# Optimization experiments

Hardware: AMD Instinct MI355X
Metric: run time of the kernel (lower is better)

The kernel has to match this reference:

```python
import jax, jax.numpy as jnp
import numpy as np

ALPHA = 0.25
GAMMA = 2.0
LOG_CLAMP = -100.0  # torch binary_cross_entropy clamps log terms at -100


def _conv_same(x, k, stride):
    # x: NHWC, k: HWIO, TF-style SAME padding
    return jax.lax.conv_general_dilated(
        x, k, window_strides=(stride, stride), padding='SAME',
        dimension_numbers=('NHWC', 'HWIO', 'NHWC'))


def _interp_axis(x, axis, out_size):
    # 1-D linear interpolation with align_corners=True semantics
    in_size = x.shape[axis]
    scale = (in_size - 1) / max(out_size - 1, 1)
    pos = jnp.arange(out_size, dtype=x.dtype) * jnp.asarray(scale, dtype=x.dtype)
    i0 = jnp.floor(pos).astype(jnp.int32)
    i1 = jnp.minimum(i0 + 1, in_size - 1)
    w = pos - i0.astype(x.dtype)
    bshape = [1] * x.ndim
    bshape[axis] = out_size
    w = w.reshape(bshape)
    return jnp.take(x, i0, axis=axis) * (1 - w) + jnp.take(x, i1, axis=axis) * w


def _upsample_bilinear_ac(x, factor):
    # NHWC bilinear upsample, align_corners=True (separable)
    x = _interp_axis(x, 1, x.shape[1] * factor)
    x = _interp_axis(x, 2, x.shape[2] * factor)
    return x


def _focal_loss_sum(p, t):
    # binary_cross_entropy (probabilities, not logits) with torch's -100 log clamp
    log_p = jnp.maximum(jnp.log(p), LOG_CLAMP)
    log_1mp = jnp.maximum(jnp.log(1.0 - p), LOG_CLAMP)
    ce = -(t * log_p + (1.0 - t) * log_1mp)
    p_t = p * t + (1.0 - p) * (1.0 - t)
    alpha_t = ALPHA * t + (1.0 - ALPHA) * (1.0 - t)
    return jnp.sum(alpha_t * ce * (1.0 - p_t) ** GAMMA)


def setup_inputs() -> dict:
    key = jax.random.key(0)
    k1, k2 = jax.random.split(key)
    B, H, W = 32, 512, 512
    network_output = jax.random.uniform(k1, (B, H, W, 1), dtype=jnp.float32)
    targets = jax.random.normal(k2, (B, H, W, 2), dtype=jnp.float32)
    # buffers (constants in the original module)
    lap2d = jnp.array([[-1.0, -1.0, -1.0], [-1.0, 8.0, -1.0], [-1.0, -1.0, -1.0]],
                      dtype=jnp.float32)
    laplacian = jnp.stack((lap2d, lap2d), axis=-1).reshape(3, 3, 2, 1)  # HWIO
    fuse_kernel = jnp.array([0.6, 0.3, 0.1], dtype=jnp.float32).reshape(1, 1, 3, 1)
    return {"network_output": network_output, "targets": targets,
            "laplacian": laplacian, "fuse_kernel": fuse_kernel}


def reference(network_output, targets, laplacian, fuse_kernel):
    t = targets[..., 0:2]                                   # [B,H,W,2]
    dt = t.dtype

    b1 = jnp.clip(_conv_same(t, laplacian, 1), 0.0, 1.0)    # [B,H,W,1]
    b1 = (b1 > 0.1).astype(dt)

    b2 = jnp.clip(_conv_same(t, laplacian, 2), 0.0, 1.0)    # [B,H/2,W/2,1]
    b2 = (_upsample_bilinear_ac(b2, 2) > 0.1).astype(dt)

    b4 = jnp.clip(_conv_same(t, laplacian, 4), 0.0, 1.0)    # [B,H/4,W/4,1]
    b4 = (_upsample_bilinear_ac(b4, 4) > 0.1).astype(dt)

    pyr = jnp.concatenate((b1, b2, b4), axis=-1)            # [B,H,W,3]
    fused = _conv_same(pyr, fuse_kernel, 1)                  # [B,H,W,1]
    fused = (fused > 0.1).astype(dt)

    return _focal_loss_sum(network_output, fused)
```

## Files before the change

kernel.cpp:

```cpp
#include <hip/hip_runtime.h>
#include <math.h>


#define B_ 32
#define H_ 512
#define W_ 512

constexpr int TY = 32;
constexpr int TX = 64;
constexpr int RRY = 37;
constexpr int SSTR = 70;
constexpr int NPAIR = RRY * 35;

__global__ __launch_bounds__(256, 8) void edge_focal_kernel(
    const float* __restrict__ net,
    const float* __restrict__ tgt,
    double* __restrict__ partial)
{
    __shared__ float sT[RRY * SSTR];
    __shared__ float sB2[18 * 36];
    __shared__ double sRed[4];

    const int tid = threadIdx.x;
    const int x0 = blockIdx.x * TX;
    const int y0 = blockIdx.y * TY;
    const int b  = blockIdx.z;

    const int lane = tid & 63;
    const int wv   = tid >> 6;
    const int py0  = wv * 8;
    const int gx   = x0 + lane;

    const float* tb = tgt + (size_t)b * (H_ * W_ * 2);
    const bool interior = (x0 >= 64) && (x0 <= 384) && (y0 >= 32) && (y0 <= 448);
    float4 q[6];
    #pragma unroll
    for (int k = 0; k < 6; ++k) {
        const int idx = tid + k * 256;
        const int r   = idx / 35;
        const int c2  = idx - r * 35;
        const int gy  = y0 - 2 + r;
        const int gxx = x0 - 2 + 2 * c2;
        const int gyc = min(max(gy, 0), H_ - 1);
        const int gxc = min(max(gxx, 0), W_ - 2);
        q[k] = *reinterpret_cast<const float4*>(tb + ((size_t)gyc * W_ + gxc) * 2);
    }

    const float* nb = net + (size_t)b * (H_ * W_);
    float p[8];
    #pragma unroll
    for (int i = 0; i < 8; ++i)
        p[i] = nb[(size_t)(y0 + py0 + i) * W_ + gx];

    #pragma unroll
    for (int k = 0; k < 6; ++k) {
        const int idx = tid + k * 256;
        if (idx < NPAIR) {
            const int r  = idx / 35;
            const int c2 = idx - r * 35;
            float v0, v1;
            if (interior) {
                v0 = q[k].x + q[k].y;
                v1 = q[k].z + q[k].w;
            } else {
                const int gy  = y0 - 2 + r;
                const int gxx = x0 - 2 + 2 * c2;
                const bool oky = (unsigned)gy < (unsigned)H_;
                v0 = (oky && (unsigned)gxx       < (unsigned)W_) ? q[k].x + q[k].y : 0.f;
                v1 = (oky && (unsigned)(gxx + 1) < (unsigned)W_) ? q[k].z + q[k].w : 0.f;
            }
            sT[r * SSTR + 2 * c2]     = v0;
            sT[r * SSTR + 2 * c2 + 1] = v1;
        }
    }
    __syncthreads();

    const float s2 = (float)(255.0 / 511.0);

    const int r2lo = (int)((float)y0 * s2);
    const int c2lo = (int)((float)x0 * s2);
    const int r2hi = min((int)((float)(y0 + TY - 1) * s2) + 1, 255);
    const int c2hi = min((int)((float)(x0 + TX - 1) * s2) + 1, 255);
    const int n2r = r2hi - r2lo + 1, n2c = c2hi - c2lo + 1;

    #pragma unroll
    for (int k = 0; k < 3; ++k) {
        const int idx = tid + k * 256;
        if (idx < 18 * 36) {
            const int rr = idx / 36, cc = idx - rr * 36;
            if (rr < n2r && cc < n2c) {
                const int ly = 2 * (r2lo + rr) - (y0 - 2);
                const int lx = 2 * (c2lo + cc) - (x0 - 2);
                const float* q0 = &sT[ly * SSTR + lx];
                const float* q1 = q0 + SSTR;
                const float* q2 = q1 + SSTR;
                float s9 = q0[0] + q0[1] + q0[2] + q1[0] + q1[1] + q1[2] + q2[0] + q2[1] + q2[2];
                float cv = 9.f * q1[1] - s9;
                sB2[idx] = fminf(fmaxf(cv, 0.f), 1.f);
            }
        }
    }
    __syncthreads();

    const int lx = lane + 2;

    const float posx = (float)gx * s2;
    const int   j0   = (int)posx;
    const int   j1   = min(j0 + 1, 255);
    const float wx   = posx - (float)j0;
    const int   bc0  = j0 - c2lo;
    const bool  xclamp = (j1 == j0);

    const float* row = &sT[(py0 + 1) * SSTR + lx - 1];
    float rs_m = row[0] + row[1] + row[2];
    row += SSTR;
    float c_c = row[1];
    float rs_c = row[0] + c_c + row[2];

    float facc = 0.f;
    #pragma unroll
    for (int i = 0; i < 8; ++i) {
        const int py = py0 + i;
        const int gy = y0 + py;
        row = &sT[(py + 3) * SSTR + lx - 1];
        const float n0 = row[0], n1 = row[1], n2 = row[2];
        const float rs_p = n0 + n1 + n2;

        const float cv1 = 9.f * c_c - (rs_m + rs_c + rs_p);
        const bool e1 = cv1 > 0.1f;

        const float posy = (float)gy * s2;
        const int   i0   = (int)posy;
        const int   i1   = min(i0 + 1, 255);
        const float wy   = posy - (float)i0;
        const int   a0   = i0 - r2lo, a1 = i1 - r2lo;
        const float v00 = sB2[a0 * 36 + bc0];
        const float v01r = sB2[a0 * 36 + bc0 + 1];
        const float v10 = sB2[a1 * 36 + bc0];
        const float v11r = sB2[a1 * 36 + bc0 + 1];
        const float v01 = xclamp ? v00 : v01r;
        const float v11 = xclamp ? v10 : v11r;
        const float ta  = v00 * (1.f - wy) + v10 * wy;
        const float tb2 = v01 * (1.f - wy) + v11 * wy;
        const float v2  = ta * (1.f - wx) + tb2 * wx;
        const bool e2 = v2 > 0.1f;

        const bool pos = e1 || e2;
        const float pv = p[i];
        const float qv = pos ? pv : 1.f - pv;
        const float al = pos ? 0.25f : 0.75f;
        const float lg = fmaxf(__logf(qv), -100.f);
        const float om = 1.f - qv;
        facc += al * (-lg) * (om * om);

        rs_m = rs_c; rs_c = rs_p; c_c = n1;
    }

    #pragma unroll
    for (int off = 32; off > 0; off >>= 1)
        facc += __shfl_down(facc, off);
    if (lane == 0) sRed[wv] = (double)facc;
    __syncthreads();
    if (tid == 0) {
        partial[((size_t)blockIdx.z * gridDim.y + blockIdx.y) * gridDim.x + blockIdx.x] =
            sRed[0] + sRed[1] + sRed[2] + sRed[3];
    }
}

__global__ __launch_bounds__(1024) void reduce_partials(
    const double* __restrict__ partial, float* __restrict__ out, int n)
{
    __shared__ double sRed[16];
    double s = 0.0;
    for (int i = threadIdx.x; i < n; i += 1024) s += partial[i];
    #pragma unroll
    for (int off = 32; off > 0; off >>= 1)
        s += __shfl_down(s, off);
    if ((threadIdx.x & 63) == 0) sRed[threadIdx.x >> 6] = s;
    __syncthreads();
    if (threadIdx.x == 0) {
        double t = 0.0;
        #pragma unroll
        for (int k = 0; k < 16; ++k) t += sRed[k];
        out[0] = (float)t;
    }
}

extern "C" void kernel_launch(void* const* d_in, const int* in_sizes, int n_in,
                              void* d_out, int out_size, void* d_ws, size_t ws_size,
                              hipStream_t stream) {
    const float* net = (const float*)d_in[0];
    const float* tgt = (const float*)d_in[1];
    double* partial = (double*)d_ws;
    float* out = (float*)d_out;

    const dim3 grid(W_ / TX, H_ / TY, B_);
    hipLaunchKernelGGL(edge_focal_kernel, grid, dim3(256), 0, stream, net, tgt, partial);
    hipLaunchKernelGGL(reduce_partials, dim3(1), dim3(1024), 0, stream,
                       partial, out, (int)(grid.x * grid.y * grid.z));
}
```

Measured before the change: 122.8 us.

## Reshape tile to 16x128 with two pixels per thread and split even/odd LDS

Changes the block tile from 32x64 to 16x128 so each thread handles two adjacent columns over 4 rows. The stride-1 stencil shares horizontal partial sums between the two pixels, and network outputs are loaded as float2. The target tile is split into even and odd column arrays in shared memory to avoid strided LDS access. Halo overhead shifts: there are fewer vertical halo rows per tile relative to its area but wider horizontal halos, and the bilinear index handling becomes more complex.

```diff
diff --git a/kernel.cpp b/kernel.cpp
--- a/kernel.cpp
+++ b/kernel.cpp
@@ -6,19 +6,21 @@
 #define H_ 512
 #define W_ 512
 
-constexpr int TY = 32;
-constexpr int TX = 64;
-constexpr int RRY = 37;
-constexpr int SSTR = 70;
-constexpr int NPAIR = RRY * 35;
+constexpr int TY = 16;
+constexpr int TX = 128;
+constexpr int RRY = 21;
+constexpr int HSTR = 68;
+constexpr int NPAIR = RRY * 67;
+constexpr int B2STR = 67;
 
 __global__ __launch_bounds__(256, 8) void edge_focal_kernel(
     const float* __restrict__ net,
     const float* __restrict__ tgt,
     double* __restrict__ partial)
 {
-    __shared__ float sT[RRY * SSTR];
-    __shared__ float sB2[18 * 36];
+    __shared__ float sTe[RRY * HSTR];
+    __shared__ float sTo[RRY * HSTR];
+    __shared__ float sB2[10 * B2STR];
     __shared__ double sRed[4];
 
     const int tid = threadIdx.x;
@@ -28,17 +30,17 @@
 
     const int lane = tid & 63;
     const int wv   = tid >> 6;
-    const int py0  = wv * 8;
-    const int gx   = x0 + lane;
+    const int py0  = wv * 4;
+    const int gx0  = x0 + 2 * lane;
 
     const float* tb = tgt + (size_t)b * (H_ * W_ * 2);
-    const bool interior = (x0 >= 64) && (x0 <= 384) && (y0 >= 32) && (y0 <= 448);
+    const bool interior = (x0 >= 128) && (x0 <= 256) && (y0 >= 16) && (y0 <= 480);
     float4 q[6];
     #pragma unroll
     for (int k = 0; k < 6; ++k) {
         const int idx = tid + k * 256;
-        const int r   = idx / 35;
-        const int c2  = idx - r * 35;
+        const int r   = idx / 67;
+        const int c2  = idx - r * 67;
         const int gy  = y0 - 2 + r;
         const int gxx = x0 - 2 + 2 * c2;
         const int gyc = min(max(gy, 0), H_ - 1);
@@ -47,17 +49,17 @@
     }
 
     const float* nb = net + (size_t)b * (H_ * W_);
-    float p[8];
-    #pragma unroll
-    for (int i = 0; i < 8; ++i)
-        p[i] = nb[(size_t)(y0 + py0 + i) * W_ + gx];
+    float2 pv[4];
+    #pragma unroll
+    for (int i = 0; i < 4; ++i)
+        pv[i] = *reinterpret_cast<const float2*>(nb + (size_t)(y0 + py0 + i) * W_ + gx0);
 
     #pragma unroll
     for (int k = 0; k < 6; ++k) {
         const int idx = tid + k * 256;
         if (idx < NPAIR) {
-            const int r  = idx / 35;
-            const int c2 = idx - r * 35;
+            const int r  = idx / 67;
+            const int c2 = idx - r * 67;
             float v0, v1;
             if (interior) {
                 v0 = q[k].x + q[k].y;
@@ -69,8 +71,8 @@
                 v0 = (oky && (unsigned)gxx       < (unsigned)W_) ? q[k].x + q[k].y : 0.f;
                 v1 = (oky && (unsigned)(gxx + 1) < (unsigned)W_) ? q[k].z + q[k].w : 0.f;
             }
-            sT[r * SSTR + 2 * c2]     = v0;
-            sT[r * SSTR + 2 * c2 + 1] = v1;
+            sTe[r * HSTR + c2] = v0;
+            sTo[r * HSTR + c2] = v1;
         }
     }
     __syncthreads();
@@ -86,75 +88,107 @@
     #pragma unroll
     for (int k = 0; k < 3; ++k) {
         const int idx = tid + k * 256;
-        if (idx < 18 * 36) {
-            const int rr = idx / 36, cc = idx - rr * 36;
+        if (idx < 10 * B2STR) {
+            const int rr = idx / B2STR, cc = idx - rr * B2STR;
             if (rr < n2r && cc < n2c) {
                 const int ly = 2 * (r2lo + rr) - (y0 - 2);
-                const int lx = 2 * (c2lo + cc) - (x0 - 2);
-                const float* q0 = &sT[ly * SSTR + lx];
-                const float* q1 = q0 + SSTR;
-                const float* q2 = q1 + SSTR;
-                float s9 = q0[0] + q0[1] + q0[2] + q1[0] + q1[1] + q1[2] + q2[0] + q2[1] + q2[2];
-                float cv = 9.f * q1[1] - s9;
+                const int e  = (2 * (c2lo + cc) - x0 + 2) >> 1;
+                const float* pe = &sTe[ly * HSTR + e];
+                const float* po = &sTo[ly * HSTR + e];
+                float s9 = pe[0] + po[0] + pe[1]
+                         + pe[HSTR] + po[HSTR] + pe[HSTR + 1]
+                         + pe[2 * HSTR] + po[2 * HSTR] + pe[2 * HSTR + 1];
+                float cv = 9.f * po[HSTR] - s9;
                 sB2[idx] = fminf(fmaxf(cv, 0.f), 1.f);
             }
         }
     }
     __syncthreads();
 
-    const int lx = lane + 2;
-
-    const float posx = (float)gx * s2;
-    const int   j0   = (int)posx;
-    const int   j1   = min(j0 + 1, 255);
-    const float wx   = posx - (float)j0;
-    const int   bc0  = j0 - c2lo;
-    const bool  xclamp = (j1 == j0);
-
-    const float* row = &sT[(py0 + 1) * SSTR + lx - 1];
-    float rs_m = row[0] + row[1] + row[2];
-    row += SSTR;
-    float c_c = row[1];
-    float rs_c = row[0] + c_c + row[2];
+    const float posx0 = (float)gx0 * s2;
+    const int   j00   = (int)posx0;
+    const float wx0   = posx0 - (float)j00;
+    const float posx1 = (float)(gx0 + 1) * s2;
+    const int   j01   = (int)posx1;
+    const float wx1   = posx1 - (float)j01;
+    const int   d     = j01 - j00;
+    const int   bc    = j00 - c2lo;
+    const bool  jc1   = (j01 == 255);
+    const float omwx0 = 1.f - wx0, omwx1 = 1.f - wx1;
+
+    const int eb = lane + 1;
+
+    float f0, f1, f2, f3;
+    #define RD4(lr) do { \
+        const float* pe_ = &sTe[(lr) * HSTR + eb]; \
+        const float* po_ = &sTo[(lr) * HSTR + lane]; \
+        f0 = po_[0]; f1 = pe_[0]; f2 = po_[1]; f3 = pe_[1]; \
+    } while (0)
+
+    RD4(py0 + 1);
+    float h0m = f0 + f1 + f2;
+    float h1m = f1 + f2 + f3;
+    RD4(py0 + 2);
+    float h0c = f0 + f1 + f2;
+    float h1c = f1 + f2 + f3;
+    float c0c = f1, c1c = f2;
 
     float facc = 0.f;
     #pragma unroll
-    for (int i = 0; i < 8; ++i) {
+    for (int i = 0; i < 4; ++i) {
         const int py = py0 + i;
         const int gy = y0 + py;
-        row = &sT[(py + 3) * SSTR + lx - 1];
-        const float n0 = row[0], n1 = row[1], n2 = row[2];
-        const float rs_p = n0 + n1 + n2;
-
-        const float cv1 = 9.f * c_c - (rs_m + rs_c + rs_p);
-        const bool e1 = cv1 > 0.1f;
+        RD4(py + 3);
+        const float h0p = f0 + f1 + f2;
+        const float h1p = f1 + f2 + f3;
+        const float n_c0 = f1, n_c1 = f2;
+
+        const float cv0 = 9.f * c0c - (h0m + h0c + h0p);
+        const float cv1 = 9.f * c1c - (h1m + h1c + h1p);
+        const bool e1_0 = cv0 > 0.1f;
+        const bool e1_1 = cv1 > 0.1f;
 
         const float posy = (float)gy * s2;
         const int   i0   = (int)posy;
         const int   i1   = min(i0 + 1, 255);
         const float wy   = posy - (float)i0;
+        const float omwy = 1.f - wy;
         const int   a0   = i0 - r2lo, a1 = i1 - r2lo;
-        const float v00 = sB2[a0 * 36 + bc0];
-        const float v01r = sB2[a0 * 36 + bc0 + 1];
-        const float v10 = sB2[a1 * 36 + bc0];
-        const float v11r = sB2[a1 * 36 + bc0 + 1];
-        const float v01 = xclamp ? v00 : v01r;
-        const float v11 = xclamp ? v10 : v11r;
-        const float ta  = v00 * (1.f - wy) + v10 * wy;
-        const float tb2 = v01 * (1.f - wy) + v11 * wy;
-        const float v2  = ta * (1.f - wx) + tb2 * wx;
-        const bool e2 = v2 > 0.1f;
-
-        const bool pos = e1 || e2;
-        const float pv = p[i];
-        const float qv = pos ? pv : 1.f - pv;
-        const float al = pos ? 0.25f : 0.75f;
-        const float lg = fmaxf(__logf(qv), -100.f);
-        const float om = 1.f - qv;
-        facc += al * (-lg) * (om * om);
-
-        rs_m = rs_c; rs_c = rs_p; c_c = n1;
-    }
+        const float w00 = sB2[a0 * B2STR + bc], w01 = sB2[a0 * B2STR + bc + 1], w02 = sB2[a0 * B2STR + bc + 2];
+        const float w10 = sB2[a1 * B2STR + bc], w11 = sB2[a1 * B2STR + bc + 1], w12 = sB2[a1 * B2STR + bc + 2];
+        const float ta = w00 * omwy + w10 * wy;
+        const float tb2 = w01 * omwy + w11 * wy;
+        const float tc = w02 * omwy + w12 * wy;
+
+        const float v2_0 = ta * omwx0 + tb2 * wx0;
+        const bool e2_0 = v2_0 > 0.1f;
+        const float lo1 = d ? tb2 : ta;
+        const float hi1 = jc1 ? lo1 : (d ? tc : tb2);
+        const float v2_1 = lo1 * omwx1 + hi1 * wx1;
+        const bool e2_1 = v2_1 > 0.1f;
+
+        {
+            const bool pos = e1_0 || e2_0;
+            const float p  = pv[i].x;
+            const float qv = pos ? p : 1.f - p;
+            const float al = pos ? 0.25f : 0.75f;
+            const float lg = fmaxf(__logf(qv), -100.f);
+            const float om = 1.f - qv;
+            facc += al * (-lg) * (om * om);
+        }
+        {
+            const bool pos = e1_1 || e2_1;
+            const float p  = pv[i].y;
+            const float qv = pos ? p : 1.f - p;
+            const float al = pos ? 0.25f : 0.75f;
+            const float lg = fmaxf(__logf(qv), -100.f);
+            const float om = 1.f - qv;
+            facc += al * (-lg) * (om * om);
+        }
+
+        h0m = h0c; h0c = h0p; h1m = h1c; h1c = h1p; c0c = n_c0; c1c = n_c1;
+    }
+    #undef RD4
 
     #pragma unroll
     for (int off = 32; off > 0; off >>= 1)
```

Measured after the change: 122.4 us. Within noise of the previous version (-0.3%).
